# Kernel tuning notes

Hardware: AMD Instinct MI355X
Metric: run time of the kernel (lower is better)

## Reference

```python
import jax, jax.numpy as jnp
import numpy as np
from jax import lax

B, S, D, F = 2, 4096, 1024, 4096
LN_EPS = 1e-6

def _layer_norm(x, scale, bias):
    mu = jnp.mean(x, axis=-1, keepdims=True)
    var = jnp.mean(jnp.square(x - mu), axis=-1, keepdims=True)
    return (x - mu) * lax.rsqrt(var + LN_EPS) * scale + bias

def _gate_loop(q, k, v, a):
    # max-headed GateLoop: one head per channel, scalar complex state per channel
    # h_t = a_t * h_{t-1} + k_t * v_t ; y_t = q_t * h_t
    kv = (k * v).astype(jnp.complex64)
    def comb(e1, e2):
        a1, x1 = e1
        a2, x2 = e2
        return (a1 * a2, a2 * x1 + x2)
    _, h = lax.associative_scan(comb, (a, kv), axis=1)
    return q.astype(jnp.complex64) * h

def setup_inputs() -> dict:
    key = jax.random.key(0)
    ks = jax.random.split(key, 12)
    sd = 1.0 / np.sqrt(D)
    sf = 1.0 / np.sqrt(F)
    return {
        "x": jax.random.normal(ks[0], (B, S, D), jnp.float32),
        "Wq": jax.random.normal(ks[1], (D, D), jnp.float32) * sd,
        "Wk": jax.random.normal(ks[2], (D, D), jnp.float32) * sd,
        "Wv": jax.random.normal(ks[3], (D, D), jnp.float32) * sd,
        "Wa": jax.random.normal(ks[4], (D, 2 * D), jnp.float32) * sd,
        "Wg": jax.random.normal(ks[5], (D, D), jnp.float32) * sd,
        "Wo": jax.random.normal(ks[6], (D, D), jnp.float32) * sd,
        "ln1_scale": jnp.ones((D,), jnp.float32),
        "ln1_bias": jnp.zeros((D,), jnp.float32),
        "W1": jax.random.normal(ks[7], (D, F), jnp.float32) * sd,
        "b1": jax.random.normal(ks[8], (F,), jnp.float32) * 1e-6,
        "W2": jax.random.normal(ks[9], (F, D), jnp.float32) * sf,
        "b2": jax.random.normal(ks[10], (D,), jnp.float32) * 1e-6,
        "ln2_scale": jnp.ones((D,), jnp.float32),
        "ln2_bias": jnp.zeros((D,), jnp.float32),
    }

def reference(x, Wq, Wk, Wv, Wa, Wg, Wo, ln1_scale, ln1_bias, W1, b1, W2, b2, ln2_scale, ln2_bias):
    q = x @ Wq
    k = x @ Wk
    v = x @ Wv
    a = x @ Wa
    a_real, a_imag = jnp.split(a, 2, axis=-1)
    a_c = a_real + 1j * a_imag
    magnitude = jnp.abs(a_c)
    phase = jnp.angle(a_c)
    a_c = jax.nn.sigmoid(magnitude).astype(jnp.complex64) * jnp.exp(1j * phase)
    g = x.astype(jnp.complex64) @ Wg.astype(jnp.complex64)
    y = _gate_loop(q, k, v, a_c)
    y = y * (g * jax.nn.sigmoid(g))  # silu on complex g
    y = y @ Wo.astype(jnp.complex64)
    y = y.real
    # dropout deterministic (training=False)
    y = _layer_norm(y + x, ln1_scale, ln1_bias)
    h = jax.nn.gelu(y @ W1 + b1)
    out = h @ W2 + b2
    out = _layer_norm(out + y, ln2_scale, ln2_bias)
    return out
```

## Files before the change

### kernel.cpp

```cpp
#include <hip/hip_runtime.h>
#include <cstdint>

typedef unsigned short u16;
typedef unsigned int u32;

#define AS1 __attribute__((address_space(1)))
#define AS3 __attribute__((address_space(3)))

typedef _Float16 f16x8 __attribute__((ext_vector_type(8)));
typedef float f32x4 __attribute__((ext_vector_type(4)));

static constexpr int Bb = 2, Ss = 4096, Dd = 1024, Ff = 4096;
static constexpr int Mtok = Bb * Ss;
static constexpr int NCH = 128;
static constexpr int TCH = Ss / NCH;
static constexpr int PW = 6144;

__device__ __forceinline__ float h2f(u16 u) {
    union { u16 u; _Float16 h; } w; w.u = u; return (float)w.h;
}
__device__ __forceinline__ u16 f2h(float f) {
    union { _Float16 h; u16 u; } w; w.h = (_Float16)f; return w.u;
}

__device__ __forceinline__ void gload_lds16(const u16* g, u16* l) {
    __builtin_amdgcn_global_load_lds((const AS1 u32*)g, (AS3 u32*)l, 16, 0, 0);
}

__global__ __launch_bounds__(256) void prep_fused(
    const float* __restrict__ x, u16* __restrict__ xb,
    const float* __restrict__ Wq, const float* __restrict__ Wk,
    const float* __restrict__ Wv, const float* __restrict__ Wa,
    const float* __restrict__ Wg, const float* __restrict__ Wo,
    const float* __restrict__ W1, const float* __restrict__ W2,
    u16* __restrict__ WTcat, u16* __restrict__ WTo,
    u16* __restrict__ WT1, u16* __restrict__ WT2) {
    __shared__ u16 t[32][33];
    const int tid = threadIdx.x;
    const int idx = blockIdx.x;
    if (idx < 8192) {
        const long i = ((long)idx * 256 + tid) * 4;
        float4 f = *(const float4*)(x + i);
        ushort4 o;
        o.x = f2h(f.x); o.y = f2h(f.y); o.z = f2h(f.z); o.w = f2h(f.w);
        *(ushort4*)(xb + i) = o;
        return;
    }
    const float* src; u16* dst; int K, N, ti;
    if (idx < 9216)       { src = Wq; dst = WTcat;             K = 1024; N = 1024; ti = idx - 8192; }
    else if (idx < 10240) { src = Wk; dst = WTcat + (1u << 20); K = 1024; N = 1024; ti = idx - 9216; }
    else if (idx < 11264) { src = Wv; dst = WTcat + (2u << 20); K = 1024; N = 1024; ti = idx - 10240; }
    else if (idx < 13312) { src = Wa; dst = WTcat + (3u << 20); K = 1024; N = 2048; ti = idx - 11264; }
    else if (idx < 14336) { src = Wg; dst = WTcat + (5u << 20); K = 1024; N = 1024; ti = idx - 13312; }
    else if (idx < 15360) { src = Wo; dst = WTo;               K = 1024; N = 1024; ti = idx - 14336; }
    else if (idx < 19456) { src = W1; dst = WT1;               K = 1024; N = 4096; ti = idx - 15360; }
    else                  { src = W2; dst = WT2;               K = 4096; N = 1024; ti = idx - 19456; }
    const int tiles_x = N >> 5;
    const int bx = ti % tiles_x, by = ti / tiles_x;
    const int n0 = bx << 5, k0 = by << 5;
    const int tx = tid & 31, ty = tid >> 5;
#pragma unroll
    for (int r = 0; r < 4; r++) {
        const int row = ty + r * 8;
        t[row][tx] = f2h(src[(long)(k0 + row) * N + n0 + tx]);
    }
    __syncthreads();
#pragma unroll
    for (int r = 0; r < 4; r++) {
        const int row = ty + r * 8;
        dst[(long)(n0 + row) * K + k0 + tx] = t[tx][row];
    }
}

template <int EPI>
__global__ __launch_bounds__(512, 2) void gemm8p(const u16* __restrict__ A,
                                                 const u16* __restrict__ BT,
                                                 u16* __restrict__ C,
                                                 const float* __restrict__ bias,
                                                 int M, int N, int K,
                                                 int lda, int ldc) {
    extern __shared__ u16 lds[];
    const int tid = threadIdx.x;

    const int ntn = N >> 8;
    const int total = (M >> 8) * ntn;
    const int tpb = total / (int)gridDim.x;
    const int cpx = total >> 3;

    const int srow = tid >> 3;
    const int scol = ((tid & 7) ^ (srow & 7)) << 3;
    const long lda64 = (long)lda << 6;
    const long ldb64 = (long)K << 6;

    const int nt = K >> 6;

    auto bases_for = [&](int t, int& tm, int& tn, const u16*& Ab, const u16*& Bb) {
        if (t > tpb - 1) t = tpb - 1;
        const int ti = (int)blockIdx.x + t * (int)gridDim.x;
        const int b = (ti & 7) * cpx + (ti >> 3);
        tm = (b / ntn) << 8;
        tn = (b % ntn) << 8;
        Ab = A + (long)(tm + srow) * lda + scol;
        Bb = BT + (long)(tn + srow) * (long)K + scol;
    };

    auto stA = [&](u16* bufbase, int h, const u16* Ab, int kt) {
        u16* d = bufbase + h * 8192 + tid * 8;
        const u16* g = Ab + (long)(h * 128) * lda + (kt << 6);
        gload_lds16(g, d);
        gload_lds16(g + lda64, d + 4096);
    };
    auto stB = [&](u16* bufbase, int h, const u16* Bb, int kt) {
        u16* d = bufbase + 16384 + h * 8192 + tid * 8;
        const u16* g = Bb + (long)(h * 128) * (long)K + (kt << 6);
        gload_lds16(g, d);
        gload_lds16(g + ldb64, d + 4096);
    };

    const int wid = tid >> 6, lane = tid & 63;
    const int r16 = lane & 15, q = lane >> 4;
    const int wm = (wid >> 2) * 128;
    const int wn = (wid & 3) * 64;
    const int r7 = r16 & 7;
    const int cx0 = (q ^ r7) << 3;
    const int cx1 = ((4 | q) ^ r7) << 3;
    const int aoff = (wm + r16) * 64;
    const int boff = 16384 + (wn + r16) * 64;

    f32x4 acc[8][4];
#pragma unroll
    for (int i = 0; i < 8; i++)
#pragma unroll
        for (int j = 0; j < 4; j++) acc[i][j] = (f32x4){0.f, 0.f, 0.f, 0.f};

    int tmc, tnc, tmn, tnn;
    const u16 *Ac, *Bc, *An, *Bn;
    bases_for(0, tmc, tnc, Ac, Bc);
    bases_for(1, tmn, tnn, An, Bn);

    stA(lds, 0, Ac, 0);
    stA(lds, 1, Ac, 0);
    stB(lds, 0, Bc, 0);
    stB(lds, 1, Bc, 0);
    stB(lds + 32768, 0, Bc, 1);
    stB(lds + 32768, 1, Bc, 1);

    for (int t = 0; t < tpb; ++t) {
        for (int it = 0; it < nt; ++it) {
            u16* sb = lds + ((it & 1) << 15);
            u16* so = lds + (((it & 1) ^ 1) << 15);

            asm volatile("s_waitcnt vmcnt(4)" ::: "memory");
            __builtin_amdgcn_s_barrier();

            f16x8 vb[4][2];
#pragma unroll
            for (int ni = 0; ni < 4; ni++) {
                vb[ni][0] = *(const f16x8*)(sb + boff + ni * 1024 + cx0);
                vb[ni][1] = *(const f16x8*)(sb + boff + ni * 1024 + cx1);
            }

#pragma unroll
            for (int p = 0; p < 4; ++p) {
                f16x8 pa[2][2];
#pragma unroll
                for (int m2 = 0; m2 < 2; m2++) {
                    pa[m2][0] = *(const f16x8*)(sb + aoff + (2 * p + m2) * 1024 + cx0);
                    pa[m2][1] = *(const f16x8*)(sb + aoff + (2 * p + m2) * 1024 + cx1);
                }
                if (p == 0) {
                    if (it + 1 < nt) stA(so, 0, Ac, it + 1);
                    else             stA(so, 0, An, 0);
                } else if (p == 1) {
                    if (it + 1 < nt) stA(so, 1, Ac, it + 1);
                    else             stA(so, 1, An, 0);
                } else if (p == 2) {
                    if (it + 2 < nt) stB(sb, 0, Bc, it + 2);
                    else             stB(sb, 0, Bn, it + 2 - nt);
                } else {
                    if (it + 2 < nt) stB(sb, 1, Bc, it + 2);
                    else             stB(sb, 1, Bn, it + 2 - nt);
                }
                __builtin_amdgcn_s_barrier();
                asm volatile("s_waitcnt lgkmcnt(0)" ::: "memory");
                __builtin_amdgcn_s_setprio(1);
#pragma unroll
                for (int m2 = 0; m2 < 2; m2++)
#pragma unroll
                    for (int ni = 0; ni < 4; ni++) {
                        acc[2 * p + m2][ni] = __builtin_amdgcn_mfma_f32_16x16x32_f16(
                            pa[m2][0], vb[ni][0], acc[2 * p + m2][ni], 0, 0, 0);
                        acc[2 * p + m2][ni] = __builtin_amdgcn_mfma_f32_16x16x32_f16(
                            pa[m2][1], vb[ni][1], acc[2 * p + m2][ni], 0, 0, 0);
                    }
                __builtin_amdgcn_s_setprio(0);
                __builtin_amdgcn_s_barrier();
            }
        }

#pragma unroll
        for (int mi = 0; mi < 8; mi++) {
#pragma unroll
            for (int ni = 0; ni < 4; ni++) {
                const int gcol = tnc + wn + ni * 16 + r16;
                float bv = 0.f;
                if (EPI) bv = bias[gcol];
#pragma unroll
                for (int j = 0; j < 4; j++) {
                    const int grow = tmc + wm + mi * 16 + q * 4 + j;
                    float v = acc[mi][ni][j];
                    if (EPI) v += bv;
                    if (EPI == 1) {
                        float tt = tanhf(0.7978845608028654f * (v + 0.044715f * v * v * v));
                        v = 0.5f * v * (1.0f + tt);
                    }
                    C[(long)grow * ldc + gcol] = f2h(v);
                    acc[mi][ni][j] = 0.f;
                }
            }
        }
        tmc = tmn; tnc = tnn; Ac = An; Bc = Bn;
        bases_for(t + 2, tmn, tnn, An, Bn);
    }

    asm volatile("s_waitcnt vmcnt(0)" ::: "memory");
}

template <int EPI>
__global__ __launch_bounds__(512, 2) void gemm8p_n128(const u16* __restrict__ A,
                                                      const u16* __restrict__ BT,
                                                      u16* __restrict__ C,
                                                      const float* __restrict__ bias,
                                                      int M, int N, int K,
                                                      int lda, int ldc) {
    extern __shared__ u16 lds[];
    const int tid = threadIdx.x;

    const int ntn = N >> 7;
    int bid = blockIdx.x;
    {
        const int cpx = gridDim.x >> 3;
        bid = (bid & 7) * cpx + (bid >> 3);
    }
    const int tm = (bid / ntn) << 8;
    const int tn = (bid % ntn) << 7;

    const int srow = tid >> 3;
    const int scol = ((tid & 7) ^ (srow & 7)) << 3;
    const u16* Abase = A + (long)(tm + srow) * lda + scol;
    const u16* Bbase = BT + (long)(tn + srow) * (long)K + scol;
    const long lda64 = (long)lda << 6;
    const long ldb64 = (long)K << 6;

    const int nt = K >> 6;

    auto stA = [&](u16* bufbase, int h, int kt) {
        u16* d = bufbase + h * 8192 + tid * 8;
        const u16* g = Abase + (long)(h * 128) * lda + (kt << 6);
        gload_lds16(g, d);
        gload_lds16(g + lda64, d + 4096);
    };
    auto stB = [&](u16* bufbase, int kt) {
        u16* d = bufbase + 16384 + tid * 8;
        const u16* g = Bbase + (kt << 6);
        gload_lds16(g, d);
        gload_lds16(g + ldb64, d + 4096);
    };

    const int wid = tid >> 6, lane = tid & 63;
    const int r16 = lane & 15, q = lane >> 4;
    const int wm = (wid >> 1) * 64;
    const int wn = (wid & 1) * 64;
    const int r7 = r16 & 7;
    const int cx0 = (q ^ r7) << 3;
    const int cx1 = ((4 | q) ^ r7) << 3;
    const int aoff = (wm + r16) * 64;
    const int boff = 16384 + (wn + r16) * 64;

    f32x4 acc[4][4];
#pragma unroll
    for (int i = 0; i < 4; i++)
#pragma unroll
        for (int j = 0; j < 4; j++) acc[i][j] = (f32x4){0.f, 0.f, 0.f, 0.f};

    {
        const int t1 = nt > 1 ? 1 : 0;
        stA(lds, 0, 0);
        stA(lds, 1, 0);
        stB(lds, 0);
        stB(lds + 24576, t1);
    }

    for (int it = 0; it < nt; ++it) {
        u16* sb = lds + (it & 1) * 24576;
        u16* so = lds + ((it & 1) ^ 1) * 24576;
        const int tA = (it + 1 < nt) ? it + 1 : nt - 1;
        const int tB = (it + 2 < nt) ? it + 2 : nt - 1;

        asm volatile("s_waitcnt vmcnt(2)" ::: "memory");
        __builtin_amdgcn_s_barrier();

        f16x8 vb[4][2];
#pragma unroll
        for (int ni = 0; ni < 4; ni++) {
            vb[ni][0] = *(const f16x8*)(sb + boff + ni * 1024 + cx0);
            vb[ni][1] = *(const f16x8*)(sb + boff + ni * 1024 + cx1);
        }

#pragma unroll
        for (int p = 0; p < 2; ++p) {
            f16x8 pa[2][2];
#pragma unroll
            for (int m2 = 0; m2 < 2; m2++) {
                pa[m2][0] = *(const f16x8*)(sb + aoff + (2 * p + m2) * 1024 + cx0);
                pa[m2][1] = *(const f16x8*)(sb + aoff + (2 * p + m2) * 1024 + cx1);
            }
            if (p == 0) {
                stA(so, 0, tA);
            } else {
                stA(so, 1, tA);
                stB(sb, tB);
            }
            __builtin_amdgcn_s_barrier();
            asm volatile("s_waitcnt lgkmcnt(0)" ::: "memory");
            __builtin_amdgcn_s_setprio(1);
#pragma unroll
            for (int m2 = 0; m2 < 2; m2++)
#pragma unroll
                for (int ni = 0; ni < 4; ni++) {
                    acc[2 * p + m2][ni] = __builtin_amdgcn_mfma_f32_16x16x32_f16(
                        pa[m2][0], vb[ni][0], acc[2 * p + m2][ni], 0, 0, 0);
                    acc[2 * p + m2][ni] = __builtin_amdgcn_mfma_f32_16x16x32_f16(
                        pa[m2][1], vb[ni][1], acc[2 * p + m2][ni], 0, 0, 0);
                }
            __builtin_amdgcn_s_setprio(0);
            __builtin_amdgcn_s_barrier();
        }
    }

    asm volatile("s_waitcnt vmcnt(0)" ::: "memory");

#pragma unroll
    for (int mi = 0; mi < 4; mi++) {
#pragma unroll
        for (int ni = 0; ni < 4; ni++) {
            const int gcol = tn + wn + ni * 16 + r16;
            float bv = 0.f;
            if (EPI) bv = bias[gcol];
#pragma unroll
            for (int j = 0; j < 4; j++) {
                const int grow = tm + wm + mi * 16 + q * 4 + j;
                float v = acc[mi][ni][j];
                if (EPI) v += bv;
                if (EPI == 1) {
                    float t = tanhf(0.7978845608028654f * (v + 0.044715f * v * v * v));
                    v = 0.5f * v * (1.0f + t);
                }
                C[(long)grow * ldc + gcol] = f2h(v);
            }
        }
    }
}

__device__ __forceinline__ void a_transform(float ar, float ai, float& cr, float& ci) {
    float m = sqrtf(ar * ar + ai * ai);
    float sg = 1.f / (1.f + __expf(-m));
    float sc = sg / fmaxf(m, 1e-30f);
    cr = ar * sc;
    ci = ai * sc;
}

__global__ __launch_bounds__(1024) void scan1(const u16* __restrict__ pcat,
                                              float4* __restrict__ sum4) {
    const int b = blockIdx.y, c = blockIdx.x, d = threadIdx.x;
    float Arp = 1.f, Aip = 0.f, Xr = 0.f, Xi = 0.f;
    const long rowbase = (long)b * Ss + (long)c * TCH;
#pragma unroll 4
    for (int s = 0; s < TCH; ++s) {
        const long ro = (rowbase + s) * PW;
        float ar = h2f(pcat[ro + 3072 + d]);
        float ai = h2f(pcat[ro + 4096 + d]);
        float kk = h2f(pcat[ro + 1024 + d]);
        float vv = h2f(pcat[ro + 2048 + d]);
        float cr, ci;
        a_transform(ar, ai, cr, ci);
        float kv = kk * vv;
        float nXr = cr * Xr - ci * Xi + kv;
        float nXi = cr * Xi + ci * Xr;
        Xr = nXr; Xi = nXi;
        float nAr = cr * Arp - ci * Aip;
        float nAi = cr * Aip + ci * Arp;
        Arp = nAr; Aip = nAi;
    }
    sum4[((long)b * NCH + c) * 1024 + d] = make_float4(Arp, Aip, Xr, Xi);
}

__global__ __launch_bounds__(256) void scan2(const float4* __restrict__ sum4,
                                             float2* __restrict__ carry) {
    const int idx = blockIdx.x * 256 + threadIdx.x;
    const int b = idx >> 10, d = idx & 1023;
    float hr = 0.f, hi = 0.f;
    for (int cb = 0; cb < NCH / 8; ++cb) {
        float4 t[8];
#pragma unroll
        for (int j = 0; j < 8; j++)
            t[j] = sum4[((long)b * NCH + cb * 8 + j) * 1024 + d];
#pragma unroll
        for (int j = 0; j < 8; j++) {
            carry[((long)b * NCH + cb * 8 + j) * 1024 + d] = make_float2(hr, hi);
            float nr = t[j].x * hr - t[j].y * hi + t[j].z;
            float ni = t[j].x * hi + t[j].y * hr + t[j].w;
            hr = nr; hi = ni;
        }
    }
}

__global__ __launch_bounds__(1024) void scan3(u16* pcat,
                                              const float2* __restrict__ carry) {
    const int b = blockIdx.y, c = blockIdx.x, d = threadIdx.x;
    float2 h0 = carry[((long)b * NCH + c) * 1024 + d];
    float hr = h0.x, hi = h0.y;
    const long rowbase = (long)b * Ss + (long)c * TCH;
#pragma unroll 4
    for (int s = 0; s < TCH; ++s) {
        const long ro = (rowbase + s) * PW;
        float ar = h2f(pcat[ro + 3072 + d]);
        float ai = h2f(pcat[ro + 4096 + d]);
        float kk = h2f(pcat[ro + 1024 + d]);
        float vv = h2f(pcat[ro + 2048 + d]);
        float cr, ci;
        a_transform(ar, ai, cr, ci);
        float kv = kk * vv;
        float nhr = cr * hr - ci * hi + kv;
        float nhi = cr * hi + ci * hr;
        hr = nhr; hi = nhi;
        float gg = h2f(pcat[ro + 5120 + d]);
        float si = gg / (1.f + __expf(-gg));
        float yv = h2f(pcat[ro + d]) * hr * si;
        pcat[ro + d] = f2h(yv);
    }
}

template <int RESF32, int OUTF32>
__global__ __launch_bounds__(256) void ln_kernel(const u16* __restrict__ a, int sa,
                                                 const void* __restrict__ bres, int sres,
                                                 const float* __restrict__ scale,
                                                 const float* __restrict__ bias,
                                                 void* __restrict__ out, int sout) {
    const int row = blockIdx.x;
    const int tid = threadIdx.x;
    const long abase = (long)row * sa;
    const long rbase = (long)row * sres;
    const long obase = (long)row * sout;
    float v[4];
#pragma unroll
    for (int j = 0; j < 4; j++) {
        int d = tid * 4 + j;
        float rb = RESF32 ? ((const float*)bres)[rbase + d]
                          : h2f(((const u16*)bres)[rbase + d]);
        v[j] = h2f(a[abase + d]) + rb;
    }
    float s = v[0] + v[1] + v[2] + v[3];
    float s2 = v[0] * v[0] + v[1] * v[1] + v[2] * v[2] + v[3] * v[3];
#pragma unroll
    for (int off = 32; off; off >>= 1) {
        s += __shfl_down(s, off);
        s2 += __shfl_down(s2, off);
    }
    __shared__ float red[8];
    const int w = tid >> 6, lane = tid & 63;
    if (lane == 0) { red[w] = s; red[4 + w] = s2; }
    __syncthreads();
    if (tid == 0) {
        float ts = red[0] + red[1] + red[2] + red[3];
        float ts2 = red[4] + red[5] + red[6] + red[7];
        float mu = ts * (1.f / 1024.f);
        float var = ts2 * (1.f / 1024.f) - mu * mu;
        red[0] = mu;
        red[1] = rsqrtf(var + 1e-6f);
    }
    __syncthreads();
    const float mu = red[0], rs = red[1];
#pragma unroll
    for (int j = 0; j < 4; j++) {
        int d = tid * 4 + j;
        float y = (v[j] - mu) * rs * scale[d] + bias[d];
        if (OUTF32) ((float*)out)[obase + d] = y;
        else        ((u16*)out)[obase + d] = f2h(y);
    }
}

extern "C" void kernel_launch(void* const* d_in, const int* in_sizes, int n_in,
                              void* d_out, int out_size, void* d_ws, size_t ws_size,
                              hipStream_t stream) {
    const float* x    = (const float*)d_in[0];
    const float* Wq   = (const float*)d_in[1];
    const float* Wk   = (const float*)d_in[2];
    const float* Wv   = (const float*)d_in[3];
    const float* Wa   = (const float*)d_in[4];
    const float* Wg   = (const float*)d_in[5];
    const float* Wo   = (const float*)d_in[6];
    const float* ln1s = (const float*)d_in[7];
    const float* ln1b = (const float*)d_in[8];
    const float* W1   = (const float*)d_in[9];
    const float* b1   = (const float*)d_in[10];
    const float* W2   = (const float*)d_in[11];
    const float* b2   = (const float*)d_in[12];
    const float* ln2s = (const float*)d_in[13];
    const float* ln2b = (const float*)d_in[14];

    u16* ws    = (u16*)d_ws;
    u16* xb    = ws;
    u16* WTcat = xb + (8u << 20);
    u16* WTo   = WTcat + (6u << 20);
    u16* WT1   = WTo + (1u << 20);
    u16* WT2   = WT1 + (4u << 20);
    u16* pcat  = WT2 + (4u << 20);

    float4* sum4  = (float4*)WTcat;
    float2* carry = (float2*)(WTcat + (2u << 20));

    static bool attr_done = false;
    if (!attr_done) {
        hipFuncSetAttribute(reinterpret_cast<const void*>(&gemm8p<0>),
                            hipFuncAttributeMaxDynamicSharedMemorySize, 131072);
        hipFuncSetAttribute(reinterpret_cast<const void*>(&gemm8p<1>),
                            hipFuncAttributeMaxDynamicSharedMemorySize, 131072);
        hipFuncSetAttribute(reinterpret_cast<const void*>(&gemm8p_n128<0>),
                            hipFuncAttributeMaxDynamicSharedMemorySize, 98304);
        hipFuncSetAttribute(reinterpret_cast<const void*>(&gemm8p_n128<2>),
                            hipFuncAttributeMaxDynamicSharedMemorySize, 98304);
        attr_done = true;
    }


    prep_fused<<<dim3(23552), dim3(256), 0, stream>>>(x, xb, Wq, Wk, Wv, Wa, Wg, Wo,
                                                      W1, W2, WTcat, WTo, WT1, WT2);

    gemm8p<0><<<dim3(256), dim3(512), 131072, stream>>>(xb, WTcat, pcat, nullptr,
                                                        Mtok, PW, 1024, 1024, PW);
    scan1<<<dim3(NCH, Bb), 1024, 0, stream>>>(pcat, sum4);
    scan2<<<dim3(8), 256, 0, stream>>>(sum4, carry);
    scan3<<<dim3(NCH, Bb), 1024, 0, stream>>>(pcat, carry);
    gemm8p_n128<0><<<dim3(256), dim3(512), 98304, stream>>>(pcat, WTo, pcat + 1024,
                                                            nullptr,
                                                            Mtok, 1024, 1024, PW, PW);
    ln_kernel<1, 0><<<dim3(Mtok), dim3(256), 0, stream>>>(pcat + 1024, PW, x, 1024,
                                                          ln1s, ln1b, pcat, PW);
    gemm8p<1><<<dim3(256), dim3(512), 131072, stream>>>(pcat, WT1, pcat + 2048, b1,
                                                        Mtok, Ff, 1024, PW, PW);
    gemm8p_n128<2><<<dim3(256), dim3(512), 98304, stream>>>(pcat + 2048, WT2,
                                                            pcat + 1024, b2,
                                                            Mtok, 1024, Ff, PW, PW);
    ln_kernel<0, 1><<<dim3(Mtok), dim3(256), 0, stream>>>(pcat + 1024, PW, pcat, PW,
                                                          ln2s, ln2b, d_out, 1024);
}
```

Measured before the change: 528.1 us.

## Vectorize scan, layernorm and transpose accesses; double scan chunks; use fast GELU

The scan kernels now have each thread handle four channels with ushort4 loads and stores, the chunk count doubles to 256, and blocks shrink to 256 threads. The layernorm kernel uses vector loads and stores, and the weight transpose writes packed 32-bit pairs. GELU's tanh form is rewritten as an equivalent sigmoid form using __expf to cut epilogue cost. These target the memory-bound scan and layernorm passes, at the cost of more per-thread register state and a larger carry buffer offset inside the workspace.

Measured after the change: 547.8 us. +3.7%, slower.

```diff
diff --git a/kernel.cpp b/kernel.cpp
--- a/kernel.cpp
+++ b/kernel.cpp
@@ -12,7 +12,7 @@
 
 static constexpr int Bb = 2, Ss = 4096, Dd = 1024, Ff = 4096;
 static constexpr int Mtok = Bb * Ss;
-static constexpr int NCH = 128;
+static constexpr int NCH = 256;
 static constexpr int TCH = Ss / NCH;
 static constexpr int PW = 6144;
 
@@ -21,6 +21,11 @@
 }
 __device__ __forceinline__ u16 f2h(float f) {
     union { _Float16 h; u16 u; } w; w.h = (_Float16)f; return w.u;
+}
+
+__device__ __forceinline__ float gelu_fast(float v) {
+    float u = 1.5957691216057308f * (v + 0.044715f * v * v * v);
+    return v / (1.f + __expf(-u));
 }
 
 __device__ __forceinline__ void gload_lds16(const u16* g, u16* l) {
@@ -65,10 +70,13 @@
         t[row][tx] = f2h(src[(long)(k0 + row) * N + n0 + tx]);
     }
     __syncthreads();
-#pragma unroll
-    for (int r = 0; r < 4; r++) {
-        const int row = ty + r * 8;
-        dst[(long)(n0 + row) * K + k0 + tx] = t[tx][row];
+    const int cx = (tid & 15) << 1;
+    const int ry = tid >> 4;
+#pragma unroll
+    for (int r = 0; r < 2; r++) {
+        const int row = ry + r * 16;
+        u32 v = (u32)t[cx][row] | ((u32)t[cx + 1][row] << 16);
+        *(u32*)(dst + (long)(n0 + row) * K + k0 + cx) = v;
     }
 }
 
@@ -210,10 +218,7 @@
                     const int grow = tmc + wm + mi * 16 + q * 4 + j;
                     float v = acc[mi][ni][j];
                     if (EPI) v += bv;
-                    if (EPI == 1) {
-                        float tt = tanhf(0.7978845608028654f * (v + 0.044715f * v * v * v));
-                        v = 0.5f * v * (1.0f + tt);
-                    }
+                    if (EPI == 1) v = gelu_fast(v);
                     C[(long)grow * ldc + gcol] = f2h(v);
                     acc[mi][ni][j] = 0.f;
                 }
@@ -352,10 +357,7 @@
                 const int grow = tm + wm + mi * 16 + q * 4 + j;
                 float v = acc[mi][ni][j];
                 if (EPI) v += bv;
-                if (EPI == 1) {
-                    float t = tanhf(0.7978845608028654f * (v + 0.044715f * v * v * v));
-                    v = 0.5f * v * (1.0f + t);
-                }
+                if (EPI == 1) v = gelu_fast(v);
                 C[(long)grow * ldc + gcol] = f2h(v);
             }
         }
@@ -370,29 +372,42 @@
     ci = ai * sc;
 }
 
-__global__ __launch_bounds__(1024) void scan1(const u16* __restrict__ pcat,
-                                              float4* __restrict__ sum4) {
-    const int b = blockIdx.y, c = blockIdx.x, d = threadIdx.x;
-    float Arp = 1.f, Aip = 0.f, Xr = 0.f, Xi = 0.f;
+__global__ __launch_bounds__(256) void scan1(const u16* __restrict__ pcat,
+                                             float4* __restrict__ sum4) {
+    const int b = blockIdx.y, c = blockIdx.x;
+    const int d0 = threadIdx.x << 2;
+    float Arp[4], Aip[4], Xr[4], Xi[4];
+#pragma unroll
+    for (int j = 0; j < 4; j++) { Arp[j] = 1.f; Aip[j] = 0.f; Xr[j] = 0.f; Xi[j] = 0.f; }
     const long rowbase = (long)b * Ss + (long)c * TCH;
-#pragma unroll 4
+#pragma unroll 2
     for (int s = 0; s < TCH; ++s) {
         const long ro = (rowbase + s) * PW;
-        float ar = h2f(pcat[ro + 3072 + d]);
-        float ai = h2f(pcat[ro + 4096 + d]);
-        float kk = h2f(pcat[ro + 1024 + d]);
-        float vv = h2f(pcat[ro + 2048 + d]);
-        float cr, ci;
-        a_transform(ar, ai, cr, ci);
-        float kv = kk * vv;
-        float nXr = cr * Xr - ci * Xi + kv;
-        float nXi = cr * Xi + ci * Xr;
-        Xr = nXr; Xi = nXi;
-        float nAr = cr * Arp - ci * Aip;
-        float nAi = cr * Aip + ci * Arp;
-        Arp = nAr; Aip = nAi;
-    }
-    sum4[((long)b * NCH + c) * 1024 + d] = make_float4(Arp, Aip, Xr, Xi);
+        ushort4 uar = *(const ushort4*)(pcat + ro + 3072 + d0);
+        ushort4 uai = *(const ushort4*)(pcat + ro + 4096 + d0);
+        ushort4 ukk = *(const ushort4*)(pcat + ro + 1024 + d0);
+        ushort4 uvv = *(const ushort4*)(pcat + ro + 2048 + d0);
+        const u16* ear = (const u16*)&uar;
+        const u16* eai = (const u16*)&uai;
+        const u16* ekk = (const u16*)&ukk;
+        const u16* evv = (const u16*)&uvv;
+#pragma unroll
+        for (int j = 0; j < 4; j++) {
+            float cr, ci;
+            a_transform(h2f(ear[j]), h2f(eai[j]), cr, ci);
+            float kv = h2f(ekk[j]) * h2f(evv[j]);
+            float nXr = cr * Xr[j] - ci * Xi[j] + kv;
+            float nXi = cr * Xi[j] + ci * Xr[j];
+            Xr[j] = nXr; Xi[j] = nXi;
+            float nAr = cr * Arp[j] - ci * Aip[j];
+            float nAi = cr * Aip[j] + ci * Arp[j];
+            Arp[j] = nAr; Aip[j] = nAi;
+        }
+    }
+    const long sbase = ((long)b * NCH + c) * 1024 + d0;
+#pragma unroll
+    for (int j = 0; j < 4; j++)
+        sum4[sbase + j] = make_float4(Arp[j], Aip[j], Xr[j], Xi[j]);
 }
 
 __global__ __launch_bounds__(256) void scan2(const float4* __restrict__ sum4,
@@ -415,29 +430,48 @@
     }
 }
 
-__global__ __launch_bounds__(1024) void scan3(u16* pcat,
-                                              const float2* __restrict__ carry) {
-    const int b = blockIdx.y, c = blockIdx.x, d = threadIdx.x;
-    float2 h0 = carry[((long)b * NCH + c) * 1024 + d];
-    float hr = h0.x, hi = h0.y;
+__global__ __launch_bounds__(256) void scan3(u16* pcat,
+                                             const float2* __restrict__ carry) {
+    const int b = blockIdx.y, c = blockIdx.x;
+    const int d0 = threadIdx.x << 2;
+    float hr[4], hi[4];
+    const long cbase = ((long)b * NCH + c) * 1024 + d0;
+#pragma unroll
+    for (int j = 0; j < 4; j++) {
+        float2 h0 = carry[cbase + j];
+        hr[j] = h0.x; hi[j] = h0.y;
+    }
     const long rowbase = (long)b * Ss + (long)c * TCH;
-#pragma unroll 4
+#pragma unroll 2
     for (int s = 0; s < TCH; ++s) {
         const long ro = (rowbase + s) * PW;
-        float ar = h2f(pcat[ro + 3072 + d]);
-        float ai = h2f(pcat[ro + 4096 + d]);
-        float kk = h2f(pcat[ro + 1024 + d]);
-        float vv = h2f(pcat[ro + 2048 + d]);
-        float cr, ci;
-        a_transform(ar, ai, cr, ci);
-        float kv = kk * vv;
-        float nhr = cr * hr - ci * hi + kv;
-        float nhi = cr * hi + ci * hr;
-        hr = nhr; hi = nhi;
-        float gg = h2f(pcat[ro + 5120 + d]);
-        float si = gg / (1.f + __expf(-gg));
-        float yv = h2f(pcat[ro + d]) * hr * si;
-        pcat[ro + d] = f2h(yv);
+        ushort4 uar = *(const ushort4*)(pcat + ro + 3072 + d0);
+        ushort4 uai = *(const ushort4*)(pcat + ro + 4096 + d0);
+        ushort4 ukk = *(const ushort4*)(pcat + ro + 1024 + d0);
+        ushort4 uvv = *(const ushort4*)(pcat + ro + 2048 + d0);
+        ushort4 ugg = *(const ushort4*)(pcat + ro + 5120 + d0);
+        ushort4 uqq = *(const ushort4*)(pcat + ro + d0);
+        const u16* ear = (const u16*)&uar;
+        const u16* eai = (const u16*)&uai;
+        const u16* ekk = (const u16*)&ukk;
+        const u16* evv = (const u16*)&uvv;
+        const u16* egg = (const u16*)&ugg;
+        const u16* eqq = (const u16*)&uqq;
+        ushort4 oy;
+        u16* ey = (u16*)&oy;
+#pragma unroll
+        for (int j = 0; j < 4; j++) {
+            float cr, ci;
+            a_transform(h2f(ear[j]), h2f(eai[j]), cr, ci);
+            float kv = h2f(ekk[j]) * h2f(evv[j]);
+            float nhr = cr * hr[j] - ci * hi[j] + kv;
+            float nhi = cr * hi[j] + ci * hr[j];
+            hr[j] = nhr; hi[j] = nhi;
+            float gg = h2f(egg[j]);
+            float si = gg / (1.f + __expf(-gg));
+            ey[j] = f2h(h2f(eqq[j]) * nhr * si);
+        }
+        *(ushort4*)(pcat + ro + d0) = oy;
     }
 }
 
@@ -452,13 +486,19 @@
     const long abase = (long)row * sa;
     const long rbase = (long)row * sres;
     const long obase = (long)row * sout;
+    const int d0 = tid * 4;
     float v[4];
-#pragma unroll
-    for (int j = 0; j < 4; j++) {
-        int d = tid * 4 + j;
-        float rb = RESF32 ? ((const float*)bres)[rbase + d]
-                          : h2f(((const u16*)bres)[rbase + d]);
-        v[j] = h2f(a[abase + d]) + rb;
+    ushort4 ua = *(const ushort4*)(a + abase + d0);
+    const u16* ea = (const u16*)&ua;
+    if (RESF32) {
+        float4 rf = *(const float4*)((const float*)bres + rbase + d0);
+        v[0] = h2f(ea[0]) + rf.x; v[1] = h2f(ea[1]) + rf.y;
+        v[2] = h2f(ea[2]) + rf.z; v[3] = h2f(ea[3]) + rf.w;
+    } else {
+        ushort4 ur = *(const ushort4*)((const u16*)bres + rbase + d0);
+        const u16* er = (const u16*)&ur;
+#pragma unroll
+        for (int j = 0; j < 4; j++) v[j] = h2f(ea[j]) + h2f(er[j]);
     }
     float s = v[0] + v[1] + v[2] + v[3];
     float s2 = v[0] * v[0] + v[1] * v[1] + v[2] * v[2] + v[3] * v[3];
@@ -481,12 +521,18 @@
     }
     __syncthreads();
     const float mu = red[0], rs = red[1];
-#pragma unroll
-    for (int j = 0; j < 4; j++) {
-        int d = tid * 4 + j;
-        float y = (v[j] - mu) * rs * scale[d] + bias[d];
-        if (OUTF32) ((float*)out)[obase + d] = y;
-        else        ((u16*)out)[obase + d] = f2h(y);
+    float4 sc = *(const float4*)(scale + d0);
+    float4 bi = *(const float4*)(bias + d0);
+    float y0 = (v[0] - mu) * rs * sc.x + bi.x;
+    float y1 = (v[1] - mu) * rs * sc.y + bi.y;
+    float y2 = (v[2] - mu) * rs * sc.z + bi.z;
+    float y3 = (v[3] - mu) * rs * sc.w + bi.w;
+    if (OUTF32) {
+        *(float4*)((float*)out + obase + d0) = make_float4(y0, y1, y2, y3);
+    } else {
+        ushort4 o;
+        o.x = f2h(y0); o.y = f2h(y1); o.z = f2h(y2); o.w = f2h(y3);
+        *(ushort4*)((u16*)out + obase + d0) = o;
     }
 }
 
@@ -518,7 +564,7 @@
     u16* pcat  = WT2 + (4u << 20);
 
     float4* sum4  = (float4*)WTcat;
-    float2* carry = (float2*)(WTcat + (2u << 20));
+    float2* carry = (float2*)(WTcat + (4u << 20));
 
     static bool attr_done = false;
     if (!attr_done) {
@@ -539,9 +585,9 @@
 
     gemm8p<0><<<dim3(256), dim3(512), 131072, stream>>>(xb, WTcat, pcat, nullptr,
                                                         Mtok, PW, 1024, 1024, PW);
-    scan1<<<dim3(NCH, Bb), 1024, 0, stream>>>(pcat, sum4);
-    scan2<<<dim3(8), 256, 0, stream>>>(sum4, carry);
-    scan3<<<dim3(NCH, Bb), 1024, 0, stream>>>(pcat, carry);
+    scan1<<<dim3(NCH, Bb), dim3(256), 0, stream>>>(pcat, sum4);
+    scan2<<<dim3(8), dim3(256), 0, stream>>>(sum4, carry);
+    scan3<<<dim3(NCH, Bb), dim3(256), 0, stream>>>(pcat, carry);
     gemm8p_n128<0><<<dim3(256), dim3(512), 98304, stream>>>(pcat, WTo, pcat + 1024,
                                                             nullptr,
                                                             Mtok, 1024, 1024, PW, PW);
```
